# Performance work log

Hardware: AMD Instinct MI355X
Metric: run time of the kernel (lower is better)

Reference implementation:

```python
import jax, jax.numpy as jnp
import numpy as np

C = 64
K = 16
DEPTH = 4            # int(sqrt(K))
N_NODES = K - 1      # 15 internal nodes per subspace tree
D = 512              # input feature dim, D // C = 8 per subspace
M = 512              # output dim (LUT rows)
N = 16384            # number of input rows


def _make_selection_matrix(C, depth=DEPTH):
    # row i within a subspace selects the transformed dim used at tree level of node i
    lvl = [0, 1, 1, 2, 2, 2, 2, 3, 3, 3, 3, 3, 3, 3, 3]
    S = np.zeros((C * N_NODES, C * depth), np.float32)
    for c in range(C):
        for i in range(N_NODES):
            S[c * N_NODES + i, c * depth + lvl[i]] = 1.0
    return S


def _make_bit_matrix(C, K=K):
    # per-subspace (K, K-1) matrix: leaf k gets +/-1 on the 4 nodes along its root-to-leaf path
    Bm = np.zeros((K, N_NODES), np.float32)
    for k in range(K):
        node = 0
        for l in range(DEPTH):
            bit = (k >> (DEPTH - 1 - l)) & 1
            Bm[k, node] = 1.0 if bit else -1.0
            node = 2 * node + 1 + bit  # children of node i are 2i+1 (left) and 2i+2 (right)
    Bfull = np.zeros((C * K, C * N_NODES), np.float32)
    for c in range(C):
        Bfull[c * K:(c + 1) * K, c * N_NODES:(c + 1) * N_NODES] = Bm
    return Bfull


def setup_inputs() -> dict:
    key = jax.random.key(0)
    k1, k2, k3, k4 = jax.random.split(key, 4)
    I = jax.random.normal(k1, (N, D), dtype=jnp.float32)
    A = jax.random.normal(k2, (C, D // C, DEPTH), dtype=jnp.float32) * (1.0 / np.sqrt(D // C))
    T = jax.random.normal(k3, (C * N_NODES,), dtype=jnp.float32) * 0.1
    L = jax.random.normal(k4, (M, C, K), dtype=jnp.float32)
    S = jnp.asarray(_make_selection_matrix(C))
    B = jnp.asarray(_make_bit_matrix(C))
    return {"I": I, "A": A, "T": T, "L": L, "S": S, "B": B}


def reference(I, A, T, L, S, B):
    C_, sub, depth = A.shape
    Kq = L.shape[-1]
    n = I.shape[0]
    # block-diagonal per-subspace projection: (n, D) -> (n, C*depth)
    Ir = I.T.reshape(C_, sub, n)                      # (C, sub, n)
    xt = jnp.einsum('csn,csd->cdn', Ir, A)            # (C, depth, n)
    xt = xt.reshape(C_ * depth, n)                    # (C*depth, n)
    # tree encoding: per-node activations, tanh relaxation, leaf scores
    h = S @ xt - T[:, None]                           # (C*15, n)
    b = (B @ jnp.tanh(h)).reshape(C_, Kq, n)          # (C, K, n)
    # straight-through hard one-hot encoding with softmax backward
    E_soft = jax.nn.softmax(b, axis=1)
    E_hard = jax.nn.one_hot(jnp.argmax(b, axis=1), Kq, axis=1, dtype=b.dtype)
    E = E_hard + E_soft - jax.lax.stop_gradient(E_soft)  # (C, K, n)
    # LUT decode: out[n, m] = sum_c L[m, c, enc(n, c)]
    out = jnp.einsum('mck,ckn->nm', L, E)
    return out
```

## Files before the change

kernel.cpp:

```cpp
#include <hip/hip_runtime.h>
#include <hip/hip_fp16.h>
#include <math.h>

#define CC 64
#define KK 16
#define NNODES 15
#define DD 512
#define MM 512
#define NN 16384

typedef _Float16 half8 __attribute__((ext_vector_type(8)));
typedef float f32x4 __attribute__((ext_vector_type(4)));
typedef unsigned long long u64;

__device__ __forceinline__ float xla_tanhf(float x) {
    const float kMax = 7.90531110763549805f;
    bool tiny = fabsf(x) < 0.0004f;
    float xc = fminf(fmaxf(x, -kMax), kMax);
    float x2 = __fmul_rn(xc, xc);
    float p = __fmaf_rn(x2, -2.76076847742355e-16f, 2.00018790482477e-13f);
    p = __fmaf_rn(x2, p, -8.60467152213735e-11f);
    p = __fmaf_rn(x2, p, 5.12229709037114e-08f);
    p = __fmaf_rn(x2, p, 1.48572235717979e-05f);
    p = __fmaf_rn(x2, p, 6.37261928875436e-04f);
    p = __fmaf_rn(x2, p, 4.89352455891786e-03f);
    p = __fmul_rn(xc, p);
    float q = __fmaf_rn(x2, 1.19825839466702e-06f, 1.18534705686654e-04f);
    q = __fmaf_rn(x2, q, 2.26843463243900e-03f);
    q = __fmaf_rn(x2, q, 4.89352518554385e-03f);
    return tiny ? x : __fdiv_rn(p, q);
}

__global__ __launch_bounds__(256) void pack_bfrag(const float* __restrict__ L,
                                                  uint4* __restrict__ Bpk) {
    const int t    = blockIdx.x * 256 + threadIdx.x;
    const int lane = t & 63;
    const int mtg  = (t >> 6) & 31;
    const int ks   = t >> 11;
    const int kbase = ks * 32 + ((lane >> 4) << 3);
    const int c     = kbase >> 4;
    const int slot0 = kbase & 15;
    const int m     = (mtg << 4) + (lane & 15);

    const float* src = L + ((size_t)m * CC + c) * KK + slot0;
    float4 v0 = ((const float4*)src)[0];
    float4 v1 = ((const float4*)src)[1];
    union { half8 h; uint4 u; } pk;
    pk.h[0] = (_Float16)v0.x; pk.h[1] = (_Float16)v0.y;
    pk.h[2] = (_Float16)v0.z; pk.h[3] = (_Float16)v0.w;
    pk.h[4] = (_Float16)v1.x; pk.h[5] = (_Float16)v1.y;
    pk.h[6] = (_Float16)v1.z; pk.h[7] = (_Float16)v1.w;
    Bpk[t] = pk.u;
}

__global__ __launch_bounds__(256, 4) void encode_kernel(const float* __restrict__ I,
                                                        const float* __restrict__ A,
                                                        const float* __restrict__ T,
                                                        unsigned* __restrict__ codesG) {
    __shared__ float sA[32 * 64];
    __shared__ float sT[CC * NNODES];

    const int tid = threadIdx.x;
    for (int i = tid; i < CC * 32; i += 256) sA[(i & 31) * 64 + (i >> 5)] = A[i];
    for (int i = tid; i < CC * NNODES; i += 256) sT[i] = T[i];
    __syncthreads();

    const int lane = tid & 63;
    const int c    = lane;
    const int w    = ((blockIdx.x & 3) << 2) + (tid >> 6);
    const int tile = blockIdx.x >> 2;
    const int n0   = tile * 64;

    float a_[32];
#pragma unroll
    for (int i = 0; i < 32; ++i) a_[i] = sA[i * 64 + c];
    float tt[NNODES];
#pragma unroll
    for (int i = 0; i < NNODES; ++i) tt[i] = sT[c * NNODES + i];

    const int lvl[NNODES] = {0, 1, 1, 2, 2, 2, 2, 3, 3, 3, 3, 3, 3, 3, 3};
    unsigned codeWord = 0;
#pragma unroll 2
    for (int rr = 0; rr < 4; ++rr) {
        const int rl = (rr << 4) + w;
        const float* Ij = I + (size_t)(n0 + rl) * DD + c * 8;
        float4 v0 = ((const float4*)Ij)[0];
        float4 v1 = ((const float4*)Ij)[1];
        float iv[8] = {v0.x, v0.y, v0.z, v0.w, v1.x, v1.y, v1.z, v1.w};

        float t[4] = {0.f, 0.f, 0.f, 0.f};
#pragma unroll
        for (int s = 0; s < 8; ++s) {
            float v = iv[s];
#pragma unroll
            for (int d = 0; d < 4; ++d)
                t[d] = __fmaf_rn(v, a_[(s << 2) + d], t[d]);
        }

        float th[NNODES];
#pragma unroll
        for (int i = 0; i < NNODES; ++i) {
            float h = __fsub_rn(t[lvl[i]], tt[i]);
            th[i] = xla_tanhf(h);
        }

        int best = 0;
        float bestv = -3.0e38f;
#pragma unroll
        for (int k = 0; k < KK; ++k) {
            int node = 0;
            float s = 0.f;
#pragma unroll
            for (int l = 0; l < 4; ++l) {
                int bit = (k >> (3 - l)) & 1;
                s = __fadd_rn(s, bit ? th[node] : -th[node]);
                node = 2 * node + 1 + bit;
            }
            if (s > bestv) { bestv = s; best = k; }
        }
        codeWord |= ((unsigned)best) << (rr << 3);
    }
    codesG[(size_t)tile * 1024 + (w << 6) + c] = codeWord;
}

#define LOADSET(S, ks_)                              \
    b##S##0 = Bp[((ks_) * 32 + 0) * 64];             \
    b##S##1 = Bp[((ks_) * 32 + 1) * 64];             \
    cw##S = cG0[(ks_) << 1];                         \
    cx##S = cG1[(ks_) << 1];

#define ONEHOT(cwv, ntb, dst) do {                                        \
    unsigned ud  = (((cwv) >> ((ntb) << 3)) & 255u) - (unsigned)sb;       \
    unsigned ud2 = ud - 4u;                                               \
    u64 lo = (ud  < 4u) ? (0x3C00ull << ((ud  & 3u) << 4)) : 0ull;        \
    u64 hi = (ud2 < 4u) ? (0x3C00ull << ((ud2 & 3u) << 4)) : 0ull;        \
    union { u64 q[2]; half8 h; } uu; uu.q[0] = lo; uu.q[1] = hi;          \
    dst = uu.h;                                                           \
} while (0)

#define COMPUTESET(S) do {                                                \
    half8 a_[8];                                                          \
    ONEHOT(cw##S, 0, a_[0]); ONEHOT(cw##S, 1, a_[1]);                     \
    ONEHOT(cw##S, 2, a_[2]); ONEHOT(cw##S, 3, a_[3]);                     \
    ONEHOT(cx##S, 0, a_[4]); ONEHOT(cx##S, 1, a_[5]);                     \
    ONEHOT(cx##S, 2, a_[6]); ONEHOT(cx##S, 3, a_[7]);                     \
    union { uint4 u; half8 h; } q0, q1;                                   \
    q0.u = b##S##0; q1.u = b##S##1;                                       \
    _Pragma("unroll")                                                     \
    for (int nt = 0; nt < 8; ++nt) {                                      \
        acc[nt][0] = __builtin_amdgcn_mfma_f32_16x16x32_f16(a_[nt], q0.h, acc[nt][0], 0, 0, 0); \
        acc[nt][1] = __builtin_amdgcn_mfma_f32_16x16x32_f16(a_[nt], q1.h, acc[nt][1], 0, 0, 0); \
    }                                                                     \
} while (0)

__global__ __launch_bounds__(256, 2) void decode_kernel(const unsigned* __restrict__ codesG,
                                                        const uint4* __restrict__ Bpk,
                                                        float* __restrict__ out) {
    const int tid = threadIdx.x;
    const int bn  = blockIdx.x >> 2;
    const int bm  = blockIdx.x & 3;
    const int n0  = bn << 7;
    const int m0  = bm << 7;

    const int w    = tid >> 6;
    const int lane = tid & 63;
    const int r15  = lane & 15;
    const int sb   = ((lane >> 4) & 1) << 3;
    const int chi  = lane >> 5;

    const uint4* Bp = Bpk + ((bm << 3) + (w << 1)) * 64 + lane;
    const unsigned* cG0 = codesG + ((size_t)(bn << 1) << 10) + (r15 << 6) + chi;
    const unsigned* cG1 = cG0 + 1024;

    f32x4 acc[8][2];
#pragma unroll
    for (int nt = 0; nt < 8; ++nt) {
        acc[nt][0] = (f32x4){0.f, 0.f, 0.f, 0.f};
        acc[nt][1] = (f32x4){0.f, 0.f, 0.f, 0.f};
    }

    uint4 bA0, bA1; unsigned cwA, cxA;
    uint4 bB0, bB1; unsigned cwB, cxB;
    uint4 bC0, bC1; unsigned cwC, cxC;
    uint4 bD0, bD1; unsigned cwD, cxD;

    LOADSET(A, 0)
    LOADSET(B, 1)
    LOADSET(C, 2)
    LOADSET(D, 3)

#pragma unroll 1
    for (int g = 0; g < 8; ++g) {
        const int ks = g << 2;
        const bool more = g < 7;
        COMPUTESET(A); if (more) { LOADSET(A, ks + 4) }
        COMPUTESET(B); if (more) { LOADSET(B, ks + 5) }
        COMPUTESET(C); if (more) { LOADSET(C, ks + 6) }
        COMPUTESET(D); if (more) { LOADSET(D, ks + 7) }
    }

    const int rbase = (lane >> 4) << 2;
#pragma unroll
    for (int nt = 0; nt < 8; ++nt) {
#pragma unroll
        for (int r = 0; r < 4; ++r) {
            float* o = out + (size_t)(n0 + (nt << 4) + rbase + r) * MM
                           + m0 + (w << 5) + r15;
            o[0]  = acc[nt][0][r];
            o[16] = acc[nt][1][r];
        }
    }
}

extern "C" void kernel_launch(void* const* d_in, const int* in_sizes, int n_in,
                              void* d_out, int out_size, void* d_ws, size_t ws_size,
                              hipStream_t stream) {
    const float* I = (const float*)d_in[0];
    const float* A = (const float*)d_in[1];
    const float* T = (const float*)d_in[2];
    const float* L = (const float*)d_in[3];

    uint4* Bpk = (uint4*)d_ws;
    unsigned* codesG = (unsigned*)((char*)d_ws + (1 << 20));
    float* out = (float*)d_out;

    hipLaunchKernelGGL(pack_bfrag, dim3(256), dim3(256), 0, stream, L, Bpk);
    hipLaunchKernelGGL(encode_kernel, dim3(1024), dim3(256), 0, stream, I, A, T, codesG);
    hipLaunchKernelGGL(decode_kernel, dim3(512), dim3(256), 0, stream, codesG, Bpk, out);
}
```

Measured before the change: 130.4 us.

## Switch decode to 32x32x16 MFMA tiles and merge pack into encode launch

The decode GEMM moves from 16x16x32 MFMA to 32x32x16 MFMA. Each wave now owns a 64x64 output block held in four f32x16 accumulators, and the B-fragment packing layout and code-word indexing are changed to match. The separate L-packing kernel is folded into the encode kernel as 256 extra blocks, which removes one launch. The larger MFMA tiles cut per-instruction overhead and one-hot construction work per FLOP, but the loop now runs twice as many k-steps, and the output stores use a new stride pattern.

New measurement: 127.0 us. 2.7% less time.

```diff
diff --git a/kernel.cpp b/kernel.cpp
--- a/kernel.cpp
+++ b/kernel.cpp
@@ -10,7 +10,7 @@
 #define NN 16384
 
 typedef _Float16 half8 __attribute__((ext_vector_type(8)));
-typedef float f32x4 __attribute__((ext_vector_type(4)));
+typedef float f32x16 __attribute__((ext_vector_type(16)));
 typedef unsigned long long u64;
 
 __device__ __forceinline__ float xla_tanhf(float x) {
@@ -31,44 +31,46 @@
     return tiny ? x : __fdiv_rn(p, q);
 }
 
-__global__ __launch_bounds__(256) void pack_bfrag(const float* __restrict__ L,
-                                                  uint4* __restrict__ Bpk) {
-    const int t    = blockIdx.x * 256 + threadIdx.x;
-    const int lane = t & 63;
-    const int mtg  = (t >> 6) & 31;
-    const int ks   = t >> 11;
-    const int kbase = ks * 32 + ((lane >> 4) << 3);
-    const int c     = kbase >> 4;
-    const int slot0 = kbase & 15;
-    const int m     = (mtg << 4) + (lane & 15);
-
-    const float* src = L + ((size_t)m * CC + c) * KK + slot0;
-    float4 v0 = ((const float4*)src)[0];
-    float4 v1 = ((const float4*)src)[1];
-    union { half8 h; uint4 u; } pk;
-    pk.h[0] = (_Float16)v0.x; pk.h[1] = (_Float16)v0.y;
-    pk.h[2] = (_Float16)v0.z; pk.h[3] = (_Float16)v0.w;
-    pk.h[4] = (_Float16)v1.x; pk.h[5] = (_Float16)v1.y;
-    pk.h[6] = (_Float16)v1.z; pk.h[7] = (_Float16)v1.w;
-    Bpk[t] = pk.u;
-}
-
-__global__ __launch_bounds__(256, 4) void encode_kernel(const float* __restrict__ I,
-                                                        const float* __restrict__ A,
-                                                        const float* __restrict__ T,
-                                                        unsigned* __restrict__ codesG) {
+__global__ __launch_bounds__(256, 4) void prep_kernel(const float* __restrict__ I,
+                                                      const float* __restrict__ A,
+                                                      const float* __restrict__ T,
+                                                      const float* __restrict__ L,
+                                                      uint4* __restrict__ Bpk,
+                                                      unsigned* __restrict__ codesG) {
     __shared__ float sA[32 * 64];
     __shared__ float sT[CC * NNODES];
 
     const int tid = threadIdx.x;
+
+    if (blockIdx.x < 256) {
+        const int t    = blockIdx.x * 256 + tid;
+        const int lane = t & 63;
+        const int mtg  = (t >> 6) & 15;
+        const int ks   = t >> 10;
+        const int col  = (mtg << 5) + (lane & 31);
+        const int slot0 = (lane >> 5) << 3;
+
+        const float* src = L + ((size_t)col * CC + ks) * KK + slot0;
+        float4 v0 = ((const float4*)src)[0];
+        float4 v1 = ((const float4*)src)[1];
+        union { half8 h; uint4 u; } pk;
+        pk.h[0] = (_Float16)v0.x; pk.h[1] = (_Float16)v0.y;
+        pk.h[2] = (_Float16)v0.z; pk.h[3] = (_Float16)v0.w;
+        pk.h[4] = (_Float16)v1.x; pk.h[5] = (_Float16)v1.y;
+        pk.h[6] = (_Float16)v1.z; pk.h[7] = (_Float16)v1.w;
+        Bpk[t] = pk.u;
+        return;
+    }
+
+    const int bid = blockIdx.x - 256;
     for (int i = tid; i < CC * 32; i += 256) sA[(i & 31) * 64 + (i >> 5)] = A[i];
     for (int i = tid; i < CC * NNODES; i += 256) sT[i] = T[i];
     __syncthreads();
 
     const int lane = tid & 63;
     const int c    = lane;
-    const int w    = ((blockIdx.x & 3) << 2) + (tid >> 6);
-    const int tile = blockIdx.x >> 2;
+    const int w    = ((bid & 3) << 2) + (tid >> 6);
+    const int tile = bid >> 2;
     const int n0   = tile * 64;
 
     float a_[32];
@@ -124,33 +126,31 @@
 }
 
 #define LOADSET(S, ks_)                              \
-    b##S##0 = Bp[((ks_) * 32 + 0) * 64];             \
-    b##S##1 = Bp[((ks_) * 32 + 1) * 64];             \
-    cw##S = cG0[(ks_) << 1];                         \
-    cx##S = cG1[(ks_) << 1];
-
-#define ONEHOT(cwv, ntb, dst) do {                                        \
-    unsigned ud  = (((cwv) >> ((ntb) << 3)) & 255u) - (unsigned)sb;       \
-    unsigned ud2 = ud - 4u;                                               \
-    u64 lo = (ud  < 4u) ? (0x3C00ull << ((ud  & 3u) << 4)) : 0ull;        \
-    u64 hi = (ud2 < 4u) ? (0x3C00ull << ((ud2 & 3u) << 4)) : 0ull;        \
-    union { u64 q[2]; half8 h; } uu; uu.q[0] = lo; uu.q[1] = hi;          \
-    dst = uu.h;                                                           \
-} while (0)
+    b##S##0 = Bp[((ks_) * 16 + 0) * 64];             \
+    b##S##1 = Bp[((ks_) * 16 + 1) * 64];             \
+    cw##S = cG[(ks_)];
 
 #define COMPUTESET(S) do {                                                \
-    half8 a_[8];                                                          \
-    ONEHOT(cw##S, 0, a_[0]); ONEHOT(cw##S, 1, a_[1]);                     \
-    ONEHOT(cw##S, 2, a_[2]); ONEHOT(cw##S, 3, a_[3]);                     \
-    ONEHOT(cx##S, 0, a_[4]); ONEHOT(cx##S, 1, a_[5]);                     \
-    ONEHOT(cx##S, 2, a_[6]); ONEHOT(cx##S, 3, a_[7]);                     \
+    const unsigned cw = cw##S;                                            \
+    half8 a0, a1;                                                         \
+    { unsigned ud  = ((cw >> sh0) & 255u) - (unsigned)sb32;               \
+      unsigned ud2 = ud - 4u;                                             \
+      u64 lo = (ud  < 4u) ? (0x3C00ull << ((ud  & 3u) << 4)) : 0ull;      \
+      u64 hi = (ud2 < 4u) ? (0x3C00ull << ((ud2 & 3u) << 4)) : 0ull;      \
+      union { u64 q[2]; half8 h; } uu; uu.q[0] = lo; uu.q[1] = hi;        \
+      a0 = uu.h; }                                                        \
+    { unsigned ud  = ((cw >> (sh0 + 16)) & 255u) - (unsigned)sb32;        \
+      unsigned ud2 = ud - 4u;                                             \
+      u64 lo = (ud  < 4u) ? (0x3C00ull << ((ud  & 3u) << 4)) : 0ull;      \
+      u64 hi = (ud2 < 4u) ? (0x3C00ull << ((ud2 & 3u) << 4)) : 0ull;      \
+      union { u64 q[2]; half8 h; } uu; uu.q[0] = lo; uu.q[1] = hi;        \
+      a1 = uu.h; }                                                        \
     union { uint4 u; half8 h; } q0, q1;                                   \
     q0.u = b##S##0; q1.u = b##S##1;                                       \
-    _Pragma("unroll")                                                     \
-    for (int nt = 0; nt < 8; ++nt) {                                      \
-        acc[nt][0] = __builtin_amdgcn_mfma_f32_16x16x32_f16(a_[nt], q0.h, acc[nt][0], 0, 0, 0); \
-        acc[nt][1] = __builtin_amdgcn_mfma_f32_16x16x32_f16(a_[nt], q1.h, acc[nt][1], 0, 0, 0); \
-    }                                                                     \
+    acc00 = __builtin_amdgcn_mfma_f32_32x32x16_f16(a0, q0.h, acc00, 0, 0, 0); \
+    acc01 = __builtin_amdgcn_mfma_f32_32x32x16_f16(a0, q1.h, acc01, 0, 0, 0); \
+    acc10 = __builtin_amdgcn_mfma_f32_32x32x16_f16(a1, q0.h, acc10, 0, 0, 0); \
+    acc11 = __builtin_amdgcn_mfma_f32_32x32x16_f16(a1, q1.h, acc11, 0, 0, 0); \
 } while (0)
 
 __global__ __launch_bounds__(256, 2) void decode_kernel(const unsigned* __restrict__ codesG,
@@ -164,25 +164,20 @@
 
     const int w    = tid >> 6;
     const int lane = tid & 63;
-    const int r15  = lane & 15;
-    const int sb   = ((lane >> 4) & 1) << 3;
-    const int chi  = lane >> 5;
-
-    const uint4* Bp = Bpk + ((bm << 3) + (w << 1)) * 64 + lane;
-    const unsigned* cG0 = codesG + ((size_t)(bn << 1) << 10) + (r15 << 6) + chi;
-    const unsigned* cG1 = cG0 + 1024;
-
-    f32x4 acc[8][2];
-#pragma unroll
-    for (int nt = 0; nt < 8; ++nt) {
-        acc[nt][0] = (f32x4){0.f, 0.f, 0.f, 0.f};
-        acc[nt][1] = (f32x4){0.f, 0.f, 0.f, 0.f};
-    }
-
-    uint4 bA0, bA1; unsigned cwA, cxA;
-    uint4 bB0, bB1; unsigned cwB, cxB;
-    uint4 bC0, bC1; unsigned cwC, cxC;
-    uint4 bD0, bD1; unsigned cwD, cxD;
+    const int wn   = w >> 1;
+    const int wm   = w & 1;
+    const int sh0  = ((lane >> 4) & 1) << 3;
+    const int sb32 = (lane >> 5) << 3;
+
+    const uint4* Bp = Bpk + ((bm << 2) + (wm << 1)) * 64 + lane;
+    const unsigned* cG = codesG + ((size_t)((bn << 1) | wn) << 10) + ((lane & 15) << 6);
+
+    f32x16 acc00 = {0.f}, acc01 = {0.f}, acc10 = {0.f}, acc11 = {0.f};
+
+    uint4 bA0, bA1; unsigned cwA;
+    uint4 bB0, bB1; unsigned cwB;
+    uint4 bC0, bC1; unsigned cwC;
+    uint4 bD0, bD1; unsigned cwD;
 
     LOADSET(A, 0)
     LOADSET(B, 1)
@@ -190,25 +185,26 @@
     LOADSET(D, 3)
 
 #pragma unroll 1
-    for (int g = 0; g < 8; ++g) {
+    for (int g = 0; g < 16; ++g) {
         const int ks = g << 2;
-        const bool more = g < 7;
+        const bool more = g < 15;
         COMPUTESET(A); if (more) { LOADSET(A, ks + 4) }
         COMPUTESET(B); if (more) { LOADSET(B, ks + 5) }
         COMPUTESET(C); if (more) { LOADSET(C, ks + 6) }
         COMPUTESET(D); if (more) { LOADSET(D, ks + 7) }
     }
 
-    const int rbase = (lane >> 4) << 2;
-#pragma unroll
-    for (int nt = 0; nt < 8; ++nt) {
-#pragma unroll
-        for (int r = 0; r < 4; ++r) {
-            float* o = out + (size_t)(n0 + (nt << 4) + rbase + r) * MM
-                           + m0 + (w << 5) + r15;
-            o[0]  = acc[nt][0][r];
-            o[16] = acc[nt][1][r];
-        }
+    const int colr = lane & 31;
+    const int rhi  = (lane >> 5) << 2;
+    const int rb0  = n0 + (wn << 6);
+    const size_t mcol = m0 + (wm << 6) + colr;
+#pragma unroll
+    for (int r = 0; r < 16; ++r) {
+        const int row = (r & 3) + ((r >> 2) << 3) + rhi;
+        out[(size_t)(rb0 + row) * MM + mcol]            = acc00[r];
+        out[(size_t)(rb0 + row) * MM + mcol + 32]       = acc01[r];
+        out[(size_t)(rb0 + 32 + row) * MM + mcol]       = acc10[r];
+        out[(size_t)(rb0 + 32 + row) * MM + mcol + 32]  = acc11[r];
     }
 }
 
@@ -224,7 +220,6 @@
     unsigned* codesG = (unsigned*)((char*)d_ws + (1 << 20));
     float* out = (float*)d_out;
 
-    hipLaunchKernelGGL(pack_bfrag, dim3(256), dim3(256), 0, stream, L, Bpk);
-    hipLaunchKernelGGL(encode_kernel, dim3(1024), dim3(256), 0, stream, I, A, T, codesG);
+    hipLaunchKernelGGL(prep_kernel, dim3(1280), dim3(256), 0, stream, I, A, T, L, Bpk, codesG);
     hipLaunchKernelGGL(decode_kernel, dim3(512), dim3(256), 0, stream, codesG, Bpk, out);
 }
```
